# Kernel tuning notes

Measured on AMD Instinct MI355X. Metric: run time of the kernel, lower is better.

## Reference

```python
import jax, jax.numpy as jnp
import numpy as np

B, S, D, F = 8, 2048, 1024, 3072
EPS = 1e-6


def _rmsnorm(x, w):
    rms = jax.lax.rsqrt(jnp.mean(x * x, axis=-1, keepdims=True) + EPS)
    return x * rms * w


def _scan_causal(x_scan, a):
    # h_t = a_t * h_{t-1} + x_t, over time axis. x_scan, a: [B,S,D]
    def step(h, inp):
        xs, at = inp
        h = at * h + xs
        return h, h
    xs_t = jnp.swapaxes(x_scan, 0, 1)  # [S,B,D]
    a_t = jnp.swapaxes(a, 0, 1)
    h0 = jnp.zeros(x_scan.shape[::2], dtype=x_scan.dtype)  # [B,D]
    _, out = jax.lax.scan(step, h0, (xs_t, a_t))
    return jnp.swapaxes(out, 0, 1)  # [B,S,D]


def setup_inputs() -> dict:
    key = jax.random.key(0)
    ks = jax.random.split(key, 12)
    sd = 1.0 / np.sqrt(D)
    sf = 1.0 / np.sqrt(F)
    return {
        "x": jax.random.normal(ks[0], (B, S, D), dtype=jnp.float32),
        "rms_mix_w": jnp.ones((D,), jnp.float32),
        "rms_ffn_w": jnp.ones((D,), jnp.float32),
        "Wg": jax.random.uniform(ks[1], (D, D), jnp.float32, -sd, sd),
        "bg": jax.random.uniform(ks[2], (D,), jnp.float32, -sd, sd),
        "Wv": jax.random.uniform(ks[3], (D, D), jnp.float32, -sd, sd),
        "bv": jax.random.uniform(ks[4], (D,), jnp.float32, -sd, sd),
        "Wd": jax.random.uniform(ks[5], (D, D), jnp.float32, -sd, sd),
        "bd": jnp.full((D,), 1.0, jnp.float32),  # decay_bias_init = 1.0
        "W_gate": jax.random.uniform(ks[6], (F, D), jnp.float32, -sd, sd),
        "W_up": jax.random.uniform(ks[7], (F, D), jnp.float32, -sd, sd),
        "W_out": jax.random.uniform(ks[8], (D, F), jnp.float32, -sf, sf),
    }


def reference(x, rms_mix_w, rms_ffn_w, Wg, bg, Wv, bv, Wd, bd, W_gate, W_up, W_out):
    # --- MinGRU mixer with pre-RMSNorm and residual ---
    xn = _rmsnorm(x, rms_mix_w)
    g = jnp.einsum("bsd,ed->bse", xn, Wg) + bg
    v = jnp.einsum("bsd,ed->bse", xn, Wv) + bv
    d = jnp.einsum("bsd,ed->bse", xn, Wd) + bd
    x_scan = jax.nn.sigmoid(g) * jnp.tanh(v)
    a = 0.001 + 0.998 * jax.nn.sigmoid(d)
    x = x + _scan_causal(x_scan, a)
    # --- SwiGLU FFN with pre-RMSNorm and residual ---
    xn = _rmsnorm(x, rms_ffn_w)
    gate = jax.nn.silu(jnp.einsum("bsd,fd->bsf", xn, W_gate))
    up = jnp.einsum("bsd,fd->bsf", xn, W_up)
    x = x + jnp.einsum("bsf,df->bsd", gate * up, W_out)
    return x
```

## Files before the change

### kernel.cpp

```cpp
#include <hip/hip_runtime.h>
#include <cstdint>
#include <cstddef>

typedef unsigned short u16;
typedef __attribute__((ext_vector_type(4))) float f32x4;
typedef __attribute__((ext_vector_type(8))) short s16x8;

#define BB 8
#define SS 2048
#define DD 1024
#define FF 3072
#define MM (BB*SS)
#define NCH 32
#define LCH (SS/NCH)

__device__ __forceinline__ float bf2f(u16 u){ union{uint32_t i;float f;}v; v.i=((uint32_t)u)<<16; return v.f; }
__device__ __forceinline__ u16 f2bf(float f){ union{float f;uint32_t i;}v; v.f=f; uint32_t r=v.i+0x7FFFu+((v.i>>16)&1u); return (u16)(r>>16); }
__device__ __forceinline__ float sigm(float x){ return 1.f/(1.f+__expf(-x)); }
__device__ __forceinline__ float tanh_f(float x){ return 2.f*sigm(2.f*x)-1.f; }

__global__ void conv_gvd(const float* __restrict__ Wg, const float* __restrict__ Wv,
                         const float* __restrict__ Wd, u16* __restrict__ out){
  size_t i = ((size_t)blockIdx.x*256 + threadIdx.x)*4;
  int row = (int)(i >> 10); int col = (int)(i & 1023);
  const float* src; int srow;
  if (row < 2048) { int grp = row >> 5, w = row & 31; src = (w < 16) ? Wg : Wv; srow = grp*16 + (w & 15); }
  else            { src = Wd; srow = row - 2048; }
  float4 v = *(const float4*)(src + (size_t)srow*1024 + col);
  ushort4 o; o.x=f2bf(v.x); o.y=f2bf(v.y); o.z=f2bf(v.z); o.w=f2bf(v.w);
  *(ushort4*)(out + i) = o;
}

__global__ void conv_gu(const float* __restrict__ Wgate, const float* __restrict__ Wup,
                        u16* __restrict__ out){
  size_t i = ((size_t)blockIdx.x*256 + threadIdx.x)*4;
  int row = (int)(i >> 10); int col = (int)(i & 1023);
  int group = row >> 5, w = row & 31;
  const float* src = (w < 16) ? Wgate : Wup;
  int srow = group*16 + (w & 15);
  float4 v = *(const float4*)(src + (size_t)srow*1024 + col);
  ushort4 o; o.x=f2bf(v.x); o.y=f2bf(v.y); o.z=f2bf(v.z); o.w=f2bf(v.w);
  *(ushort4*)(out + i) = o;
}

__global__ void conv_cp(const float* __restrict__ W, u16* __restrict__ out){
  size_t i = ((size_t)blockIdx.x*256 + threadIdx.x)*4;
  float4 v = *(const float4*)(W + i);
  ushort4 o; o.x=f2bf(v.x); o.y=f2bf(v.y); o.z=f2bf(v.z); o.w=f2bf(v.w);
  *(ushort4*)(out + i) = o;
}

__global__ void rmsnorm_k(const float* __restrict__ x, const float* __restrict__ wgt,
                          u16* __restrict__ out){
  const int row = blockIdx.x, t = threadIdx.x;
  float4 v = ((const float4*)(x + (size_t)row*DD))[t];
  float ss = v.x*v.x + v.y*v.y + v.z*v.z + v.w*v.w;
  #pragma unroll
  for (int o = 32; o > 0; o >>= 1) ss += __shfl_down(ss, o, 64);
  __shared__ float sacc[4];
  if ((t & 63) == 0) sacc[t >> 6] = ss;
  __syncthreads();
  float tot = sacc[0] + sacc[1] + sacc[2] + sacc[3];
  float r = rsqrtf(tot * (1.f/(float)DD) + 1e-6f);
  float4 wv = ((const float4*)wgt)[t];
  ushort4 o; o.x=f2bf(v.x*r*wv.x); o.y=f2bf(v.y*r*wv.y); o.z=f2bf(v.z*r*wv.z); o.w=f2bf(v.w*r*wv.w);
  ((ushort4*)(out + (size_t)row*DD))[t] = o;
}

template<int EPI, int NTN>
__global__ __launch_bounds__(512) void gemm256(
    const u16* __restrict__ A, const u16* __restrict__ Bm, int K,
    const float* __restrict__ bg, const float* __restrict__ bv, const float* __restrict__ bd,
    u16* __restrict__ o_xs, float* __restrict__ o_a,
    u16* __restrict__ o_h, float* __restrict__ o_y)
{
  __shared__ u16 lds[2*32768];
  const int tid = threadIdx.x, w = tid >> 6, l = tid & 63;
  const int wr = w >> 2, wc = w & 3;
  const int bid = blockIdx.x;
  const int xcd = bid & 7, p = bid >> 3;
  const int g = p >> 5, q = p & 31;
  const int tm = xcd*8 + (q >> 2);
  const int tn = (q & 3) + (g << 2);

  const int srow  = w*8 + (l >> 3);
  const int sslot = (l & 7) ^ ((l >> 3) & 7);
  const u16* gA = A  + (size_t)(tm*256 + srow)*K + sslot*8;
  const u16* gB = Bm + (size_t)(tn*256 + srow)*K + sslot*8;

#define STAGE_HALF(dbuf, isB, h, tile) do { \
    const u16* gsrc_ = ((isB) ? gB : gA) + ((size_t)(h)*128)*K + (size_t)(tile)*64; \
    u16* ldst_ = &lds[(dbuf)*32768 + (isB)*16384 + (h)*8192 + w*512]; \
    __builtin_amdgcn_global_load_lds((const __attribute__((address_space(1))) void*)gsrc_, \
        (__attribute__((address_space(3))) void*)ldst_, 16, 0, 0); \
    __builtin_amdgcn_global_load_lds((const __attribute__((address_space(1))) void*)(gsrc_ + (size_t)64*K), \
        (__attribute__((address_space(3))) void*)(ldst_ + 4096), 16, 0, 0); \
  } while(0)

  const int aRow = wr*128 + (l & 15);
  const int bRow = wc*64  + (l & 15);
  const int sl0  = (((l >> 4) ^ (l & 7))) * 8;

#define LDA(cb, mi, ks) (*(const s16x8*)&lds[(cb)*32768 + (aRow + (mi)*16)*64 + (sl0 ^ ((ks)*32))])
#define LDB(cb, ni, ks) (*(const s16x8*)&lds[(cb)*32768 + 16384 + (bRow + (ni)*16)*64 + (sl0 ^ ((ks)*32))])

#define LOADB(cb) do { \
    bfr[0][0]=LDB(cb,0,0); bfr[0][1]=LDB(cb,0,1); \
    bfr[1][0]=LDB(cb,1,0); bfr[1][1]=LDB(cb,1,1); \
    bfr[2][0]=LDB(cb,2,0); bfr[2][1]=LDB(cb,2,1); \
    bfr[3][0]=LDB(cb,3,0); bfr[3][1]=LDB(cb,3,1); \
  } while(0)

#define PHASE(cb, mi0, STAGE_STMT, ...) do { \
    s16x8 a00 = LDA(cb, (mi0),   0), a01 = LDA(cb, (mi0),   1); \
    s16x8 a10 = LDA(cb, (mi0)+1, 0), a11 = LDA(cb, (mi0)+1, 1); \
    STAGE_STMT; \
    __builtin_amdgcn_s_barrier(); \
    asm volatile("s_waitcnt lgkmcnt(0)" ::: "memory"); \
    __builtin_amdgcn_s_setprio(1); \
    acc[(mi0)  ][0] = __builtin_amdgcn_mfma_f32_16x16x32_bf16(a00, bfr[0][0], acc[(mi0)  ][0],0,0,0); \
    acc[(mi0)  ][1] = __builtin_amdgcn_mfma_f32_16x16x32_bf16(a00, bfr[1][0], acc[(mi0)  ][1],0,0,0); \
    acc[(mi0)  ][2] = __builtin_amdgcn_mfma_f32_16x16x32_bf16(a00, bfr[2][0], acc[(mi0)  ][2],0,0,0); \
    acc[(mi0)  ][3] = __builtin_amdgcn_mfma_f32_16x16x32_bf16(a00, bfr[3][0], acc[(mi0)  ][3],0,0,0); \
    acc[(mi0)+1][0] = __builtin_amdgcn_mfma_f32_16x16x32_bf16(a10, bfr[0][0], acc[(mi0)+1][0],0,0,0); \
    acc[(mi0)+1][1] = __builtin_amdgcn_mfma_f32_16x16x32_bf16(a10, bfr[1][0], acc[(mi0)+1][1],0,0,0); \
    acc[(mi0)+1][2] = __builtin_amdgcn_mfma_f32_16x16x32_bf16(a10, bfr[2][0], acc[(mi0)+1][2],0,0,0); \
    acc[(mi0)+1][3] = __builtin_amdgcn_mfma_f32_16x16x32_bf16(a10, bfr[3][0], acc[(mi0)+1][3],0,0,0); \
    acc[(mi0)  ][0] = __builtin_amdgcn_mfma_f32_16x16x32_bf16(a01, bfr[0][1], acc[(mi0)  ][0],0,0,0); \
    acc[(mi0)  ][1] = __builtin_amdgcn_mfma_f32_16x16x32_bf16(a01, bfr[1][1], acc[(mi0)  ][1],0,0,0); \
    acc[(mi0)  ][2] = __builtin_amdgcn_mfma_f32_16x16x32_bf16(a01, bfr[2][1], acc[(mi0)  ][2],0,0,0); \
    acc[(mi0)  ][3] = __builtin_amdgcn_mfma_f32_16x16x32_bf16(a01, bfr[3][1], acc[(mi0)  ][3],0,0,0); \
    acc[(mi0)+1][0] = __builtin_amdgcn_mfma_f32_16x16x32_bf16(a11, bfr[0][1], acc[(mi0)+1][0],0,0,0); \
    acc[(mi0)+1][1] = __builtin_amdgcn_mfma_f32_16x16x32_bf16(a11, bfr[1][1], acc[(mi0)+1][1],0,0,0); \
    acc[(mi0)+1][2] = __builtin_amdgcn_mfma_f32_16x16x32_bf16(a11, bfr[2][1], acc[(mi0)+1][2],0,0,0); \
    acc[(mi0)+1][3] = __builtin_amdgcn_mfma_f32_16x16x32_bf16(a11, bfr[3][1], acc[(mi0)+1][3],0,0,0); \
    __builtin_amdgcn_s_setprio(0); \
    __VA_ARGS__; \
    __builtin_amdgcn_s_barrier(); \
  } while(0)

  f32x4 acc[8][4] = {};
  s16x8 bfr[4][2];
  const int nk = K >> 6;

  STAGE_HALF(0,0,0,0); STAGE_HALF(0,0,1,0);
  STAGE_HALF(0,1,0,0); STAGE_HALF(0,1,1,0);
  STAGE_HALF(1,1,0,1); STAGE_HALF(1,1,1,1);
  asm volatile("s_waitcnt vmcnt(4)" ::: "memory");
  __builtin_amdgcn_s_barrier();

  for (int it = 0, t = 0; it < (nk >> 1); ++it, t += 2) {
    const int tp1 = t + 1;
    int tp2 = t + 2; if (tp2 >= nk) tp2 -= nk;
    int tp3 = t + 3; if (tp3 >= nk) tp3 -= nk;
    LOADB(0);
    PHASE(0, 0, STAGE_HALF(1,0,0,tp1), );
    PHASE(0, 2, STAGE_HALF(1,0,1,tp1), );
    PHASE(0, 4, STAGE_HALF(0,1,0,tp2), );
    PHASE(0, 6, STAGE_HALF(0,1,1,tp2), asm volatile("s_waitcnt vmcnt(4)" ::: "memory"));
    LOADB(1);
    PHASE(1, 0, STAGE_HALF(0,0,0,tp2), );
    PHASE(1, 2, STAGE_HALF(0,0,1,tp2), );
    PHASE(1, 4, STAGE_HALF(1,1,0,tp3), );
    PHASE(1, 6, STAGE_HALF(1,1,1,tp3), asm volatile("s_waitcnt vmcnt(4)" ::: "memory"));
  }
#undef PHASE
#undef LOADB
#undef LDA
#undef LDB
#undef STAGE_HALF

  const int rb = tm*256 + wr*128 + ((l >> 4) << 2);
  const int lc = l & 15;
  if constexpr (EPI == 0) {
    if (tn < 8) {
      #pragma unroll
      for (int mi = 0; mi < 8; ++mi)
        #pragma unroll
        for (int j = 0; j < 2; ++j) {
          int f = tn*128 + wc*32 + j*16 + lc;
          float bgf = bg[f], bvf = bv[f];
          #pragma unroll
          for (int i = 0; i < 4; ++i) {
            int r = rb + mi*16 + i;
            float g2 = acc[mi][2*j][i]   + bgf;
            float v2 = acc[mi][2*j+1][i] + bvf;
            o_xs[(size_t)r*DD + f] = f2bf(sigm(g2) * tanh_f(v2));
          }
        }
    } else {
      #pragma unroll
      for (int mi = 0; mi < 8; ++mi)
        #pragma unroll
        for (int ni = 0; ni < 4; ++ni) {
          int c = (tn-8)*256 + wc*64 + ni*16 + lc;
          float bdc = bd[c];
          #pragma unroll
          for (int i = 0; i < 4; ++i) {
            int r = rb + mi*16 + i;
            o_a[(size_t)r*DD + c] = 0.001f + 0.998f*sigm(acc[mi][ni][i] + bdc);
          }
        }
    }
  } else if constexpr (EPI == 1) {
    #pragma unroll
    for (int mi = 0; mi < 8; ++mi)
      #pragma unroll
      for (int j = 0; j < 2; ++j) {
        int f = tn*128 + wc*32 + j*16 + lc;
        #pragma unroll
        for (int i = 0; i < 4; ++i) {
          int r = rb + mi*16 + i;
          float g2 = acc[mi][2*j][i], u2 = acc[mi][2*j+1][i];
          o_h[(size_t)r*FF + f] = f2bf(g2 * sigm(g2) * u2);
        }
      }
  } else {
    #pragma unroll
    for (int mi = 0; mi < 8; ++mi)
      #pragma unroll
      for (int ni = 0; ni < 4; ++ni) {
        int c = tn*256 + wc*64 + ni*16 + lc;
        #pragma unroll
        for (int i = 0; i < 4; ++i) {
          int r = rb + mi*16 + i;
          size_t idx = (size_t)r*DD + c;
          o_y[idx] = o_y[idx] + acc[mi][ni][i];
        }
      }
  }
}

__global__ void scan_pass1(const u16* __restrict__ xs, const float* __restrict__ ab,
                           float* __restrict__ Ac, float* __restrict__ Xc){
  const int bid = blockIdx.x;
  const int d = ((bid & 3) << 8) + threadIdx.x;
  const int c = (bid >> 2) & (NCH-1);
  const int b = bid >> 7;
  size_t base = ((size_t)b*SS + (size_t)c*LCH)*DD + d;
  float A = 1.f, X = 0.f;
  for (int tt = 0; tt < LCH; ++tt){
    size_t idx = base + (size_t)tt*DD;
    float a = ab[idx];
    X = a*X + bf2f(xs[idx]); A *= a;
  }
  size_t o = ((size_t)b*NCH + c)*DD + d;
  Ac[o] = A; Xc[o] = X;
}

__global__ void scan_pass2(const float* __restrict__ Ac, const float* __restrict__ Xc,
                           float* __restrict__ hin){
  int gid = blockIdx.x*256 + threadIdx.x;
  int b = gid >> 10, d = gid & 1023;
  float h = 0.f;
  for (int c = 0; c < NCH; ++c){
    size_t o = ((size_t)b*NCH + c)*DD + d;
    hin[o] = h;
    h = Ac[o]*h + Xc[o];
  }
}

__global__ void scan_pass3(const u16* __restrict__ xs, const float* __restrict__ ab,
                           const float* __restrict__ hin,
                           const float* __restrict__ x, float* __restrict__ y){
  const int bid = blockIdx.x;
  const int d = ((bid & 3) << 8) + threadIdx.x;
  const int c = (bid >> 2) & (NCH-1);
  const int b = bid >> 7;
  size_t base = ((size_t)b*SS + (size_t)c*LCH)*DD + d;
  float h = hin[((size_t)b*NCH + c)*DD + d];
  for (int tt = 0; tt < LCH; ++tt){
    size_t idx = base + (size_t)tt*DD;
    float a = ab[idx];
    h = a*h + bf2f(xs[idx]);
    y[idx] = x[idx] + h;
  }
}

extern "C" void kernel_launch(void* const* d_in, const int* in_sizes, int n_in,
                              void* d_out, int out_size, void* d_ws, size_t ws_size,
                              hipStream_t stream) {
  const float* x     = (const float*)d_in[0];
  const float* rmw   = (const float*)d_in[1];
  const float* rfw   = (const float*)d_in[2];
  const float* Wg    = (const float*)d_in[3];
  const float* bg    = (const float*)d_in[4];
  const float* Wv    = (const float*)d_in[5];
  const float* bv    = (const float*)d_in[6];
  const float* Wd    = (const float*)d_in[7];
  const float* bd    = (const float*)d_in[8];
  const float* Wgate = (const float*)d_in[9];
  const float* Wup   = (const float*)d_in[10];
  const float* Wout  = (const float*)d_in[11];
  float* out = (float*)d_out;

  char* p = (char*)d_ws;
  u16*  xn    = (u16*)p;              p += (size_t)MM*DD*2;
  u16*  Wgvd  = (u16*)p;              p += (size_t)3072*1024*2;
  u16*  Wgu   = (u16*)p;              p += (size_t)6144*1024*2;
  u16*  Wo    = (u16*)p;              p += (size_t)1024*3072*2;
  char* big   = p;                    p += (size_t)MM*FF*2;
  u16*  xs    = (u16*)big;
  float* ab   = (float*)(big + (size_t)MM*DD*2);
  u16*  hbuf  = (u16*)big;
  float* Ac   = (float*)p;            p += (size_t)BB*NCH*DD*4;
  float* Xc   = (float*)p;            p += (size_t)BB*NCH*DD*4;
  float* hin  = (float*)p;            p += (size_t)BB*NCH*DD*4;

  conv_gvd<<<3072, 256, 0, stream>>>(Wg, Wv, Wd, Wgvd);
  conv_gu <<<6144, 256, 0, stream>>>(Wgate, Wup, Wgu);
  conv_cp <<<3072, 256, 0, stream>>>(Wout, Wo);

  rmsnorm_k<<<MM, 256, 0, stream>>>(x, rmw, xn);
  gemm256<0,12><<<64*12, 512, 0, stream>>>(xn, Wgvd, 1024,
      bg, bv, bd, xs, ab, nullptr, nullptr);
  scan_pass1<<<BB*NCH*4, 256, 0, stream>>>(xs, ab, Ac, Xc);
  scan_pass2<<<32, 256, 0, stream>>>(Ac, Xc, hin);
  scan_pass3<<<BB*NCH*4, 256, 0, stream>>>(xs, ab, hin, x, out);

  rmsnorm_k<<<MM, 256, 0, stream>>>(out, rfw, xn);
  gemm256<1,24><<<64*24, 512, 0, stream>>>(xn, Wgu, 1024,
      nullptr, nullptr, nullptr, nullptr, nullptr, hbuf, nullptr);
  gemm256<2,4><<<64*4, 512, 0, stream>>>(hbuf, Wo, 3072,
      nullptr, nullptr, nullptr, nullptr, nullptr, nullptr, out);
}
```

Measured before the change: 546.3 us.

## Fuse scan pass3 with FFN RMSNorm, store decay in bf16, rework GEMM tile mapping

Scan pass 3 now has each block process whole 1024-wide rows for one chunk, so it can also compute the FFN RMSNorm and write the bf16 normalized activations directly. This removes the separate rmsnorm launch and its reread of the fp32 residual. The decay tensor `a` is stored as bf16 instead of fp32, halving its write and read traffic, at some cost in recurrence precision. The chunk count doubles to 64 to keep enough blocks in flight, and the GEMM tile mapping changes to a generic XCD-strided row-major order.

Measured after the change: 532.3 us. 1.03x faster.

```diff
diff --git a/kernel.cpp b/kernel.cpp
--- a/kernel.cpp
+++ b/kernel.cpp
@@ -11,7 +11,7 @@
 #define DD 1024
 #define FF 3072
 #define MM (BB*SS)
-#define NCH 32
+#define NCH 64
 #define LCH (SS/NCH)
 
 __device__ __forceinline__ float bf2f(u16 u){ union{uint32_t i;float f;}v; v.i=((uint32_t)u)<<16; return v.f; }
@@ -71,17 +71,15 @@
 __global__ __launch_bounds__(512) void gemm256(
     const u16* __restrict__ A, const u16* __restrict__ Bm, int K,
     const float* __restrict__ bg, const float* __restrict__ bv, const float* __restrict__ bd,
-    u16* __restrict__ o_xs, float* __restrict__ o_a,
+    u16* __restrict__ o_xs, u16* __restrict__ o_a,
     u16* __restrict__ o_h, float* __restrict__ o_y)
 {
   __shared__ u16 lds[2*32768];
   const int tid = threadIdx.x, w = tid >> 6, l = tid & 63;
   const int wr = w >> 2, wc = w & 3;
-  const int bid = blockIdx.x;
-  const int xcd = bid & 7, p = bid >> 3;
-  const int g = p >> 5, q = p & 31;
-  const int tm = xcd*8 + (q >> 2);
-  const int tn = (q & 3) + (g << 2);
+  const int nwg = gridDim.x, bid = blockIdx.x;
+  const int sw = (bid & 7) * (nwg >> 3) + (bid >> 3);
+  const int tm = sw / NTN, tn = sw % NTN;
 
   const int srow  = w*8 + (l >> 3);
   const int sslot = (l & 7) ^ ((l >> 3) & 7);
@@ -198,7 +196,7 @@
           #pragma unroll
           for (int i = 0; i < 4; ++i) {
             int r = rb + mi*16 + i;
-            o_a[(size_t)r*DD + c] = 0.001f + 0.998f*sigm(acc[mi][ni][i] + bdc);
+            o_a[(size_t)r*DD + c] = f2bf(0.001f + 0.998f*sigm(acc[mi][ni][i] + bdc));
           }
         }
     }
@@ -231,17 +229,17 @@
   }
 }
 
-__global__ void scan_pass1(const u16* __restrict__ xs, const float* __restrict__ ab,
+__global__ void scan_pass1(const u16* __restrict__ xs, const u16* __restrict__ ab,
                            float* __restrict__ Ac, float* __restrict__ Xc){
   const int bid = blockIdx.x;
   const int d = ((bid & 3) << 8) + threadIdx.x;
   const int c = (bid >> 2) & (NCH-1);
-  const int b = bid >> 7;
+  const int b = bid >> 8;
   size_t base = ((size_t)b*SS + (size_t)c*LCH)*DD + d;
   float A = 1.f, X = 0.f;
   for (int tt = 0; tt < LCH; ++tt){
     size_t idx = base + (size_t)tt*DD;
-    float a = ab[idx];
+    float a = bf2f(ab[idx]);
     X = a*X + bf2f(xs[idx]); A *= a;
   }
   size_t o = ((size_t)b*NCH + c)*DD + d;
@@ -260,20 +258,45 @@
   }
 }
 
-__global__ void scan_pass3(const u16* __restrict__ xs, const float* __restrict__ ab,
-                           const float* __restrict__ hin,
-                           const float* __restrict__ x, float* __restrict__ y){
+__global__ __launch_bounds__(256) void scan_pass3_norm(
+    const u16* __restrict__ xs, const u16* __restrict__ ab,
+    const float* __restrict__ hin, const float* __restrict__ x,
+    const float* __restrict__ rfw, float* __restrict__ y, u16* __restrict__ xn)
+{
   const int bid = blockIdx.x;
-  const int d = ((bid & 3) << 8) + threadIdx.x;
-  const int c = (bid >> 2) & (NCH-1);
-  const int b = bid >> 7;
-  size_t base = ((size_t)b*SS + (size_t)c*LCH)*DD + d;
-  float h = hin[((size_t)b*NCH + c)*DD + d];
+  const int c = bid & (NCH-1);
+  const int b = bid >> 6;
+  const int t = threadIdx.x;
+  float h[4], w[4];
+  size_t hb = ((size_t)b*NCH + c)*DD + t;
+  #pragma unroll
+  for (int j = 0; j < 4; ++j){ h[j] = hin[hb + j*256]; w[j] = rfw[t + j*256]; }
+  __shared__ float sred[4];
+  size_t base = ((size_t)b*SS + (size_t)c*LCH)*DD + t;
   for (int tt = 0; tt < LCH; ++tt){
-    size_t idx = base + (size_t)tt*DD;
-    float a = ab[idx];
-    h = a*h + bf2f(xs[idx]);
-    y[idx] = x[idx] + h;
+    size_t rowb = base + (size_t)tt*DD;
+    float yv[4]; float ss = 0.f;
+    #pragma unroll
+    for (int j = 0; j < 4; ++j){
+      size_t idx = rowb + (size_t)j*256;
+      float a = bf2f(ab[idx]);
+      h[j] = a*h[j] + bf2f(xs[idx]);
+      yv[j] = x[idx] + h[j];
+      y[idx] = yv[j];
+      ss += yv[j]*yv[j];
+    }
+    #pragma unroll
+    for (int o = 32; o > 0; o >>= 1) ss += __shfl_down(ss, o, 64);
+    if ((t & 63) == 0) sred[t >> 6] = ss;
+    __syncthreads();
+    float tot = sred[0] + sred[1] + sred[2] + sred[3];
+    float r = rsqrtf(tot * (1.f/(float)DD) + 1e-6f);
+    #pragma unroll
+    for (int j = 0; j < 4; ++j){
+      size_t idx = rowb + (size_t)j*256;
+      xn[idx] = f2bf(yv[j]*r*w[j]);
+    }
+    __syncthreads();
   }
 }
 
@@ -301,7 +324,7 @@
   u16*  Wo    = (u16*)p;              p += (size_t)1024*3072*2;
   char* big   = p;                    p += (size_t)MM*FF*2;
   u16*  xs    = (u16*)big;
-  float* ab   = (float*)(big + (size_t)MM*DD*2);
+  u16*  ab    = (u16*)(big + (size_t)MM*DD*2);
   u16*  hbuf  = (u16*)big;
   float* Ac   = (float*)p;            p += (size_t)BB*NCH*DD*4;
   float* Xc   = (float*)p;            p += (size_t)BB*NCH*DD*4;
@@ -316,9 +339,8 @@
       bg, bv, bd, xs, ab, nullptr, nullptr);
   scan_pass1<<<BB*NCH*4, 256, 0, stream>>>(xs, ab, Ac, Xc);
   scan_pass2<<<32, 256, 0, stream>>>(Ac, Xc, hin);
-  scan_pass3<<<BB*NCH*4, 256, 0, stream>>>(xs, ab, hin, x, out);
-
-  rmsnorm_k<<<MM, 256, 0, stream>>>(out, rfw, xn);
+  scan_pass3_norm<<<BB*NCH, 256, 0, stream>>>(xs, ab, hin, x, rfw, out, xn);
+
   gemm256<1,24><<<64*24, 512, 0, stream>>>(xn, Wgu, 1024,
       nullptr, nullptr, nullptr, nullptr, nullptr, hbuf, nullptr);
   gemm256<2,4><<<64*4, 512, 0, stream>>>(hbuf, Wo, 3072,
```
